# Performance work log

Hardware: AMD Instinct MI355X
Metric: run time of the kernel (lower is better)

## Reference

```python
import jax, jax.numpy as jnp
import numpy as np

HEAD_DIM = 128
N_HEADS = 32
N_KV_HEADS = 8
ROPE_BASE = 500000.0
QK_EPS = 1e-6


def _rope_cos_sin(position_ids, head_dim, base, dtype):
    # position_ids: [B, S] int -> cos/sin [B, 1, S, head_dim]
    inv_freq = 1.0 / (base ** (jnp.arange(0, head_dim, 2, dtype=jnp.float32) / head_dim))
    freqs = position_ids.astype(jnp.float32)[..., None] * inv_freq  # [B, S, D/2]
    emb = jnp.concatenate([freqs, freqs], axis=-1)  # [B, S, D]
    return jnp.cos(emb).astype(dtype)[:, None], jnp.sin(emb).astype(dtype)[:, None]


def _rotate_half(x):
    x1, x2 = jnp.split(x, 2, axis=-1)
    return jnp.concatenate([-x2, x1], axis=-1)


def _qk_norm(x, scale, eps):
    # L2 norm (not RMS): scale * x / (||x||_2 + eps)
    norm = jnp.sqrt(jnp.sum(x * x, axis=-1, keepdims=True))
    return scale * x / (norm + eps)


def setup_inputs() -> dict:
    key = jax.random.key(0)
    ks = jax.random.split(key, 7)
    B, S, H = 1, 2048, 4096
    kv_dim = N_KV_HEADS * HEAD_DIM
    return {
        "hidden_states": jax.random.normal(ks[0], (B, S, H), dtype=jnp.float32),
        "position_ids": jnp.broadcast_to(jnp.arange(S, dtype=jnp.int64 if jax.config.jax_enable_x64 else jnp.int32), (B, S)),
        "Wq": jax.random.normal(ks[1], (H, H), dtype=jnp.float32) * (H ** -0.5),
        "Wk": jax.random.normal(ks[2], (kv_dim, H), dtype=jnp.float32) * (H ** -0.5),
        "Wv": jax.random.normal(ks[3], (kv_dim, H), dtype=jnp.float32) * (H ** -0.5),
        "Wo": jax.random.normal(ks[4], (H, H), dtype=jnp.float32) * (H ** -0.5),
        "q_scale": jnp.ones((HEAD_DIM,), dtype=jnp.float32),
        "k_scale": jnp.ones((HEAD_DIM,), dtype=jnp.float32),
    }


def reference(hidden_states, position_ids, Wq, Wk, Wv, Wo, q_scale, k_scale):
    B, S, H = hidden_states.shape
    scaling = 1.0 / np.sqrt(HEAD_DIM)

    # projections (torch Linear: y = x @ W.T)
    q = (hidden_states @ Wq.T).reshape(B, S, N_HEADS, HEAD_DIM).transpose(0, 2, 1, 3)
    k = (hidden_states @ Wk.T).reshape(B, S, N_KV_HEADS, HEAD_DIM).transpose(0, 2, 1, 3)
    v = (hidden_states @ Wv.T).reshape(B, S, N_KV_HEADS, HEAD_DIM).transpose(0, 2, 1, 3)

    cos, sin = _rope_cos_sin(position_ids, HEAD_DIM, ROPE_BASE, q.dtype)
    q = q * cos + _rotate_half(q) * sin
    k = k * cos + _rotate_half(k) * sin

    q = _qk_norm(q, q_scale, QK_EPS)
    k = _qk_norm(k, k_scale, QK_EPS)

    # GQA: repeat kv heads to match query heads
    n_rep = N_HEADS // N_KV_HEADS
    k = jnp.repeat(k, n_rep, axis=1)  # [B, n_heads, S, D]
    v = jnp.repeat(v, n_rep, axis=1)

    # causal SDPA
    scores = jnp.einsum("bhqd,bhkd->bhqk", q, k) * scaling
    causal = jnp.tril(jnp.ones((S, S), dtype=bool))
    scores = jnp.where(causal, scores, jnp.finfo(scores.dtype).min)
    attn = jax.nn.softmax(scores, axis=-1)
    out = jnp.einsum("bhqk,bhkd->bhqd", attn, v)  # [B, H, S, D]

    out = out.transpose(0, 2, 1, 3).reshape(B, S, H)
    return out @ Wo.T
```

## Files before the change

### kernel.cpp

```cpp
#include <hip/hip_runtime.h>
#include <math.h>

typedef unsigned short u16;
typedef unsigned int u32;
typedef __attribute__((ext_vector_type(8))) short bf16x8;
typedef __attribute__((ext_vector_type(4))) float f32x4;

#define S_LEN 2048
#define HID 4096
#define NH 32
#define NKV 8
#define HD 128
#define QS 6144

__device__ __forceinline__ u16 f2bf(float f) {
  u32 u = __float_as_uint(f);
  u32 r = (u + 0x7FFFu + ((u >> 16) & 1u)) >> 16;
  return (u16)r;
}
__device__ __forceinline__ float bf2f(u16 v) {
  return __uint_as_float(((u32)v) << 16);
}
__device__ __forceinline__ f32x4 mfma16(bf16x8 a, bf16x8 b, f32x4 c) {
  return __builtin_amdgcn_mfma_f32_16x16x32_bf16(a, b, c, 0, 0, 0);
}
__device__ __forceinline__ void async16(const u16* g, u16* l) {
  __builtin_amdgcn_global_load_lds(
      (__attribute__((address_space(1))) void*)g,
      (__attribute__((address_space(3))) void*)l, 16, 0, 0);
}
#if __has_builtin(__builtin_amdgcn_exp2f)
#define EXP2(x) __builtin_amdgcn_exp2f(x)
#else
#define EXP2(x) exp2f(x)
#endif

__global__ __launch_bounds__(256) void conv_all(
    const float* __restrict__ hs, const float* __restrict__ wq,
    const float* __restrict__ wk, const float* __restrict__ wv,
    const float* __restrict__ wo, u16* __restrict__ dhs, u16* __restrict__ dwq,
    u16* __restrict__ dwk, u16* __restrict__ dwv, u16* __restrict__ dwo) {
  int i = blockIdx.x * 256 + threadIdx.x;
  const float* src;
  u16* dst;
  int off;
  if (i < 2097152) { src = hs; dst = dhs; off = 0; }
  else if (i < 6291456) { src = wq; dst = dwq; off = 2097152; }
  else if (i < 7340032) { src = wk; dst = dwk; off = 6291456; }
  else if (i < 8388608) { src = wv; dst = dwv; off = 7340032; }
  else { src = wo; dst = dwo; off = 8388608; }
  int j = i - off;
  float4 v = ((const float4*)src)[j];
  ushort4 o;
  o.x = f2bf(v.x); o.y = f2bf(v.y); o.z = f2bf(v.z); o.w = f2bf(v.w);
  ((ushort4*)dst)[j] = o;
}


#define VMC(n) asm volatile("s_waitcnt vmcnt(" #n ")" ::: "memory")

#define LDA(qi, d)                                                         \
  {                                                                        \
    const u16* p_ = As + (d)*16384 + (wm * 128 + (qi)*64 + cl) * 64;       \
    _Pragma("unroll") for (int ii = 0; ii < 4; ii++)                       \
        _Pragma("unroll") for (int kk = 0; kk < 2; kk++)                   \
            a0[ii][kk] =                                                   \
        *(const bf16x8*)(p_ + ii * 1024 + ((c0 ^ (kk << 2)) << 3));        \
  }

#define LDB(dst, qj, d)                                                    \
  {                                                                        \
    const u16* p_ = Bs + (d)*16384 + (wn * 64 + (qj)*32 + cl) * 64;        \
    _Pragma("unroll") for (int jj = 0; jj < 2; jj++)                       \
        _Pragma("unroll") for (int kk = 0; kk < 2; kk++)                   \
            dst[jj][kk] =                                                  \
        *(const bf16x8*)(p_ + jj * 1024 + ((c0 ^ (kk << 2)) << 3));        \
  }

#define MM(qi, qj, bsrc)                                                   \
  {                                                                        \
    _Pragma("unroll") for (int ii = 0; ii < 4; ii++)                       \
        _Pragma("unroll") for (int jj = 0; jj < 2; jj++)                   \
            _Pragma("unroll") for (int kk = 0; kk < 2; kk++)               \
                acc[(qi)*4 + ii][(qj)*2 + jj] =                            \
        mfma16(a0[ii][kk], bsrc[jj][kk], acc[(qi)*4 + ii][(qj)*2 + jj]);   \
  }

#define PH(MMA)                                                  \
  {                                                              \
    __builtin_amdgcn_s_barrier();                                \
    asm volatile("s_waitcnt lgkmcnt(0)" ::: "memory");           \
    __builtin_amdgcn_sched_barrier(0);                           \
    __builtin_amdgcn_s_setprio(1);                               \
    MMA;                                                         \
    __builtin_amdgcn_s_setprio(0);                               \
    __builtin_amdgcn_sched_barrier(0);                           \
    __builtin_amdgcn_s_barrier();                                \
  }

__global__ __launch_bounds__(512, 2) void gemm256(
    const u16* __restrict__ A, const u16* __restrict__ B,
    u16* __restrict__ Cb, float* __restrict__ Cf, int N, int K) {
  extern __shared__ u16 lds[];
  u16* As = lds;
  u16* Bs = lds + 32768;
  const int tid = threadIdx.x;
  const int lane = tid & 63, wv = tid >> 6;
  const int cl = lane & 15, qd = lane >> 4;
  const int wm = wv >> 2, wn = wv & 3;
  const int c0 = qd ^ (cl & 7);

  const int cpx = gridDim.x >> 3;
  const int swz = (blockIdx.x & 7) * cpx + (blockIdx.x >> 3);
  const int m0 = (swz & 7) * 256;
  const int n0 = (swz >> 3) * 256;

  u32 aof[2][2], bof[2][2];
#pragma unroll
  for (int h = 0; h < 2; h++)
#pragma unroll
    for (int q = 0; q < 2; q++) {
      int g = q * 512 + wv * 64 + lane;
      int r = h * 128 + (g >> 3);
      int c = (g & 7) ^ (r & 7);
      aof[h][q] = (u32)(m0 + r) * K + c * 8;
      bof[h][q] = (u32)(n0 + r) * K + c * 8;
    }
  u16* asb = As + wv * 512;
  u16* bsb = Bs + wv * 512;

  f32x4 acc[8][4];
  f32x4 zz = {0.f, 0.f, 0.f, 0.f};
#pragma unroll
  for (int i = 0; i < 8; i++)
#pragma unroll
    for (int j = 0; j < 4; j++) acc[i][j] = zz;
  bf16x8 a0[4][2], b0[2][2], b1[2][2];

  const int NT = K >> 6;

  {
    auto sh = [&](const u16* g, const u32* off, int t, u16* dst) {
      async16(g + (size_t)t * 64 + off[0], dst);
      async16(g + (size_t)t * 64 + off[1], dst + 4096);
    };
    sh(A, aof[0], 0, asb);
    sh(A, aof[1], 0, asb + 8192);
    sh(B, bof[0], 0, bsb);
    sh(B, bof[1], 0, bsb + 8192);
    sh(B, bof[0], 1, bsb + 16384);
    sh(B, bof[1], 1, bsb + 16384 + 8192);
  }
  VMC(4);
  __builtin_amdgcn_sched_barrier(0);
  __builtin_amdgcn_s_barrier();

  for (int it = 0; it < (NT >> 1); ++it) {
    const int t = it * 2;
    const bool s2 = (t + 2) < NT;
    auto sh = [&](const u16* g, const u32* off, int tt, u16* dst) {
      async16(g + (size_t)tt * 64 + off[0], dst);
      async16(g + (size_t)tt * 64 + off[1], dst + 4096);
    };
    LDA(0, 0); LDB(b0, 0, 0);
    sh(A, aof[0], t + 1, asb + 16384);
    PH(MM(0, 0, b0));
    LDB(b1, 1, 0);
    sh(A, aof[1], t + 1, asb + 16384 + 8192);
    PH(MM(0, 1, b1));
    LDA(1, 0);
    if (s2) sh(B, bof[0], t + 2, bsb);
    PH(MM(1, 0, b0));
    if (s2) {
      sh(B, bof[1], t + 2, bsb + 8192);
      VMC(4);
    } else {
      VMC(0);
    }
    PH(MM(1, 1, b1));
    LDA(0, 1); LDB(b0, 0, 1);
    if (s2) sh(A, aof[0], t + 2, asb);
    PH(MM(0, 0, b0));
    LDB(b1, 1, 1);
    if (s2) sh(A, aof[1], t + 2, asb + 8192);
    PH(MM(0, 1, b1));
    LDA(1, 1);
    if (s2) sh(B, bof[0], t + 3, bsb + 16384);
    PH(MM(1, 0, b0));
    if (s2) sh(B, bof[1], t + 3, bsb + 16384 + 8192);
    VMC(4);
    PH(MM(1, 1, b1));
  }

#pragma unroll
  for (int i = 0; i < 8; i++)
#pragma unroll
    for (int j = 0; j < 4; j++) {
      int row = m0 + wm * 128 + i * 16 + qd * 4;
      int col = n0 + wn * 64 + j * 16 + cl;
#pragma unroll
      for (int r = 0; r < 4; r++) {
        float v = acc[i][j][r];
        if (Cb) Cb[(size_t)(row + r) * N + col] = f2bf(v);
        else    Cf[(size_t)(row + r) * N + col] = v;
      }
    }
}

__global__ __launch_bounds__(256) void rope_l2norm(
    u16* __restrict__ x, const int* __restrict__ pos_ids,
    const float* __restrict__ scale, int hmask, int hshift, int stride) {
  const int lane = threadIdx.x & 63;
  const int wv = threadIdx.x >> 6;
  const int idx = blockIdx.x * 4 + wv;
  const int s = idx >> hshift;
  const int h = idx & hmask;
  u16* p = x + (size_t)s * stride + h * HD;
  const float pos = (float)pos_ids[s];
  const float inv = expf((float)lane * -0.20503692777194264f);
  float sn, cs;
  sincosf(pos * inv, &sn, &cs);
  float a = bf2f(p[lane]);
  float b = bf2f(p[lane + 64]);
  float ra = a * cs - b * sn;
  float rb = b * cs + a * sn;
  float ss = ra * ra + rb * rb;
#pragma unroll
  for (int off = 32; off >= 1; off >>= 1) ss += __shfl_xor(ss, off, 64);
  float rd = 1.0f / (sqrtf(ss) + 1e-6f);
  p[lane] = f2bf(scale[lane] * ra * rd);
  p[lane + 64] = f2bf(scale[lane + 64] * rb * rd);
}

__global__ __launch_bounds__(256) void transpose_v(const u16* __restrict__ v,
                                                   u16* __restrict__ vt) {
  __shared__ u16 t[64][65];
  const int r = threadIdx.x >> 6;
  const int c = threadIdx.x & 63;
  const int s0 = blockIdx.x * 64, d0 = blockIdx.y * 64;
#pragma unroll
  for (int i = 0; i < 16; i++) {
    int row = i * 4 + r;
    t[row][c] = v[(size_t)(s0 + row) * QS + d0 + c];
  }
  __syncthreads();
#pragma unroll
  for (int i = 0; i < 16; i++) {
    int row = i * 4 + r;
    vt[(size_t)(d0 + row) * S_LEN + s0 + c] = t[c][row];
  }
}

#define PLD 68

__global__ __launch_bounds__(512) void flash_attn(
    const u16* __restrict__ QKV, const u16* __restrict__ Vt,
    u16* __restrict__ O) {
  __shared__ u16 Ks[64 * 128];
  __shared__ u16 Vs[128 * 64];
  __shared__ u16 Ps[128 * PLD];
  const int tid = threadIdx.x;
  const int lane = tid & 63, wv = tid >> 6;
  const int cl = lane & 15, qd = lane >> 4;
  const int qbi = blockIdx.x, h = blockIdx.y;
  const int q0 = qbi * 128, kvh = h >> 2;
  const float es = 0.12751629240081506f;

  bf16x8 aQ[4];
  {
    const u16* qrow = QKV + (size_t)(q0 + wv * 16 + cl) * QS + h * HD + qd * 8;
#pragma unroll
    for (int kk = 0; kk < 4; kk++) aQ[kk] = *(const bf16x8*)(qrow + kk * 32);
  }

  f32x4 oacc[8];
  f32x4 zz = {0.f, 0.f, 0.f, 0.f};
#pragma unroll
  for (int n = 0; n < 8; n++) oacc[n] = zz;
  float lsum[4] = {0.f, 0.f, 0.f, 0.f};

  const u16* Kbase = QKV + 4096 + kvh * HD;
  const u16* Vbase = Vt + (size_t)kvh * HD * S_LEN;

  const int row_min = q0 + wv * 16;
  const int ktmax = 2 * qbi + 1;

  for (int kt = 0; kt <= ktmax; kt++) {
    __syncthreads();
#pragma unroll
    for (int q = 0; q < 2; q++) {
      int c = q * 512 + wv * 64 + lane;
      int kr = c >> 4, kg = (c & 15) ^ (kr & 15);
      async16(Kbase + (size_t)(kt * 64 + kr) * QS + kg * 8,
              Ks + (q * 512 + wv * 64) * 8);
      int vr = c >> 3, vg = (c & 7) ^ (vr & 7);
      async16(Vbase + (size_t)vr * S_LEN + kt * 64 + vg * 8,
              Vs + (q * 512 + wv * 64) * 8);
    }
    __syncthreads();

    if (kt * 64 <= row_min + 15) {
      f32x4 sacc[4];
#pragma unroll
      for (int j = 0; j < 4; j++) sacc[j] = zz;
#pragma unroll
      for (int j = 0; j < 4; j++) {
        int row = j * 16 + cl;
#pragma unroll
        for (int kk = 0; kk < 4; kk++) {
          int ch = (kk * 4 + qd) ^ (row & 15);
          bf16x8 bK = *(const bf16x8*)&Ks[row * 128 + ch * 8];
          sacc[j] = mfma16(aQ[kk], bK, sacc[j]);
        }
      }

      float pm[4][4];
      if (kt * 64 + 63 > row_min) {
        const int grow = row_min + qd * 4;
#pragma unroll
        for (int j = 0; j < 4; j++) {
          int gcol = kt * 64 + j * 16 + cl;
#pragma unroll
          for (int r = 0; r < 4; r++)
            pm[j][r] = (gcol <= grow + r) ? EXP2(sacc[j][r] * es) : 0.f;
        }
      } else {
#pragma unroll
        for (int j = 0; j < 4; j++)
#pragma unroll
          for (int r = 0; r < 4; r++) pm[j][r] = EXP2(sacc[j][r] * es);
      }
#pragma unroll
      for (int j = 0; j < 4; j++)
#pragma unroll
        for (int r = 0; r < 4; r++) lsum[r] += pm[j][r];

#pragma unroll
      for (int j = 0; j < 4; j++)
#pragma unroll
        for (int r = 0; r < 4; r++)
          Ps[(wv * 16 + qd * 4 + r) * PLD + j * 16 + cl] = f2bf(pm[j][r]);
      __asm__ volatile("s_waitcnt lgkmcnt(0)" ::: "memory");

#pragma unroll
      for (int kk = 0; kk < 2; kk++) {
        bf16x8 aP = *(const bf16x8*)&Ps[(wv * 16 + cl) * PLD + kk * 32 + qd * 8];
#pragma unroll
        for (int n = 0; n < 8; n++) {
          int row = n * 16 + cl;
          int ch = (kk * 4 + qd) ^ (row & 7);
          bf16x8 bV = *(const bf16x8*)&Vs[row * 64 + ch * 8];
          oacc[n] = mfma16(aP, bV, oacc[n]);
        }
      }
    }
  }

#pragma unroll
  for (int r = 0; r < 4; r++) {
#pragma unroll
    for (int off = 8; off >= 1; off >>= 1) lsum[r] += __shfl_xor(lsum[r], off, 64);
  }
#pragma unroll
  for (int r = 0; r < 4; r++) {
    float il = 1.0f / lsum[r];
    int row = row_min + qd * 4 + r;
#pragma unroll
    for (int n = 0; n < 8; n++)
      O[(size_t)row * HID + h * HD + n * 16 + cl] = f2bf(oacc[n][r] * il);
  }
}

extern "C" void kernel_launch(void* const* d_in, const int* in_sizes, int n_in,
                              void* d_out, int out_size, void* d_ws, size_t ws_size,
                              hipStream_t stream) {
  const float* hs = (const float*)d_in[0];
  const int* pos = (const int*)d_in[1];
  const float* Wq = (const float*)d_in[2];
  const float* Wk = (const float*)d_in[3];
  const float* Wv = (const float*)d_in[4];
  const float* Wo = (const float*)d_in[5];
  const float* qsc = (const float*)d_in[6];
  const float* ksc = (const float*)d_in[7];
  float* out = (float*)d_out;
  char* ws = (char*)d_ws;
  const size_t MB = 1u << 20;

  u16* hs_b  = (u16*)(ws + 0 * MB);
  u16* wq_b  = (u16*)(ws + 16 * MB);
  u16* wk_b  = (u16*)(ws + 48 * MB);
  u16* wv_b  = (u16*)(ws + 56 * MB);
  u16* qkv_b = (u16*)(ws + 64 * MB);
  u16* vt_b  = (u16*)(ws + 88 * MB);
  u16* wo_b  = (u16*)(ws + 92 * MB);
  u16* o_b   = hs_b;

  static bool attr_set = false;
  if (!attr_set) {
    hipFuncSetAttribute(reinterpret_cast<const void*>(gemm256),
                        hipFuncAttributeMaxDynamicSharedMemorySize, 131072);
    attr_set = true;
  }

  conv_all<<<49152, 256, 0, stream>>>(hs, Wq, Wk, Wv, Wo,
                                      hs_b, wq_b, wk_b, wv_b, wo_b);

  gemm256<<<dim3((S_LEN / 256) * (QS / 256)), 512, 131072, stream>>>(
      hs_b, wq_b, qkv_b, nullptr, QS, HID);

  rope_l2norm<<<S_LEN * NH / 4, 256, 0, stream>>>(qkv_b, pos, qsc, NH - 1, 5, QS);
  rope_l2norm<<<S_LEN * NKV / 4, 256, 0, stream>>>(qkv_b + 4096, pos, ksc, NKV - 1, 3, QS);
  transpose_v<<<dim3(S_LEN / 64, (NKV * HD) / 64), 256, 0, stream>>>(qkv_b + 5120, vt_b);

  flash_attn<<<dim3(S_LEN / 128, NH), 512, 0, stream>>>(qkv_b, vt_b, o_b);

  gemm256<<<dim3((S_LEN / 256) * (HID / 256)), 512, 131072, stream>>>(
      o_b, wo_b, nullptr, out, HID, HID);
}
```

Before: 516.8 us.

## Shrink GEMM tiles for more blocks and pair causal attention query blocks

The GEMM kernel is templated on N-tile width (256x192 for the QKV projection, 256x128 for the output projection) with a 4x2 wave layout. This raises the block count to fill more compute units and lowers LDS per block, at the cost of less data reuse per tile. Flash attention now runs each block over two query tiles, i and 15-i, so every block does the same causal amount of work. This removes the triangular load imbalance but halves the grid to 256 blocks.

```diff
diff --git a/kernel.cpp b/kernel.cpp
--- a/kernel.cpp
+++ b/kernel.cpp
@@ -61,8 +61,8 @@
 
 #define LDA(qi, d)                                                         \
   {                                                                        \
-    const u16* p_ = As + (d)*16384 + (wm * 128 + (qi)*64 + cl) * 64;       \
-    _Pragma("unroll") for (int ii = 0; ii < 4; ii++)                       \
+    const u16* p_ = As + (d)*16384 + (wm * 64 + (qi)*32 + cl) * 64;        \
+    _Pragma("unroll") for (int ii = 0; ii < 2; ii++)                       \
         _Pragma("unroll") for (int kk = 0; kk < 2; kk++)                   \
             a0[ii][kk] =                                                   \
         *(const bf16x8*)(p_ + ii * 1024 + ((c0 ^ (kk << 2)) << 3));        \
@@ -70,8 +70,9 @@
 
 #define LDB(dst, qj, d)                                                    \
   {                                                                        \
-    const u16* p_ = Bs + (d)*16384 + (wn * 64 + (qj)*32 + cl) * 64;        \
-    _Pragma("unroll") for (int jj = 0; jj < 2; jj++)                       \
+    const u16* p_ =                                                        \
+        Bs + (d)*BSTR + (wn * (BN / 2) + (qj) * (BN / 4) + cl) * 64;       \
+    _Pragma("unroll") for (int jj = 0; jj < NJ; jj++)                      \
         _Pragma("unroll") for (int kk = 0; kk < 2; kk++)                   \
             dst[jj][kk] =                                                  \
         *(const bf16x8*)(p_ + jj * 1024 + ((c0 ^ (kk << 2)) << 3));        \
@@ -79,11 +80,11 @@
 
 #define MM(qi, qj, bsrc)                                                   \
   {                                                                        \
-    _Pragma("unroll") for (int ii = 0; ii < 4; ii++)                       \
-        _Pragma("unroll") for (int jj = 0; jj < 2; jj++)                   \
+    _Pragma("unroll") for (int ii = 0; ii < 2; ii++)                       \
+        _Pragma("unroll") for (int jj = 0; jj < NJ; jj++)                  \
             _Pragma("unroll") for (int kk = 0; kk < 2; kk++)               \
-                acc[(qi)*4 + ii][(qj)*2 + jj] =                            \
-        mfma16(a0[ii][kk], bsrc[jj][kk], acc[(qi)*4 + ii][(qj)*2 + jj]);   \
+                acc[(qi)*2 + ii][(qj)*NJ + jj] = mfma16(                   \
+                    a0[ii][kk], bsrc[jj][kk], acc[(qi)*2 + ii][(qj)*NJ + jj]); \
   }
 
 #define PH(MMA)                                                  \
@@ -98,106 +99,116 @@
     __builtin_amdgcn_s_barrier();                                \
   }
 
-__global__ __launch_bounds__(512, 2) void gemm256(
+#define VMCNJ()                       \
+  {                                   \
+    if constexpr (NJ == 2) VMC(2);    \
+    else VMC(3);                      \
+  }
+
+template <int NJ>
+__global__ __launch_bounds__(512, 2) void gemm8p(
     const u16* __restrict__ A, const u16* __restrict__ B,
     u16* __restrict__ Cb, float* __restrict__ Cf, int N, int K) {
+  constexpr int BN = NJ * 64;
+  constexpr int BSTR = BN * 64;
   extern __shared__ u16 lds[];
   u16* As = lds;
   u16* Bs = lds + 32768;
   const int tid = threadIdx.x;
   const int lane = tid & 63, wv = tid >> 6;
   const int cl = lane & 15, qd = lane >> 4;
-  const int wm = wv >> 2, wn = wv & 3;
+  const int wm = wv >> 1, wn = wv & 1;
   const int c0 = qd ^ (cl & 7);
 
   const int cpx = gridDim.x >> 3;
   const int swz = (blockIdx.x & 7) * cpx + (blockIdx.x >> 3);
   const int m0 = (swz & 7) * 256;
-  const int n0 = (swz >> 3) * 256;
-
-  u32 aof[2][2], bof[2][2];
-#pragma unroll
-  for (int h = 0; h < 2; h++)
-#pragma unroll
-    for (int q = 0; q < 2; q++) {
-      int g = q * 512 + wv * 64 + lane;
-      int r = h * 128 + (g >> 3);
-      int c = (g & 7) ^ (r & 7);
-      aof[h][q] = (u32)(m0 + r) * K + c * 8;
-      bof[h][q] = (u32)(n0 + r) * K + c * 8;
-    }
-  u16* asb = As + wv * 512;
-  u16* bsb = Bs + wv * 512;
-
-  f32x4 acc[8][4];
+  const int n0 = (swz >> 3) * BN;
+
+  u32 aof[4], bof[NJ];
+#pragma unroll
+  for (int q = 0; q < 4; q++) {
+    int r = q * 64 + wv * 8 + (lane >> 3);
+    int c = (lane & 7) ^ (r & 7);
+    aof[q] = (u32)(m0 + r) * K + c * 8;
+  }
+#pragma unroll
+  for (int q = 0; q < NJ; q++) {
+    int r = q * 64 + wv * 8 + (lane >> 3);
+    int c = (lane & 7) ^ (r & 7);
+    bof[q] = (u32)(n0 + r) * K + c * 8;
+  }
+  const int sbo = wv * 512;
+
+  auto STA = [&](int t, int d, int ra) {
+    async16(A + (size_t)t * 64 + aof[ra], As + d * 16384 + ra * 4096 + sbo);
+  };
+  auto STB = [&](int t, int d, int rb) {
+    async16(B + (size_t)t * 64 + bof[rb], Bs + d * BSTR + rb * 4096 + sbo);
+  };
+
+  f32x4 acc[4][2 * NJ];
   f32x4 zz = {0.f, 0.f, 0.f, 0.f};
 #pragma unroll
-  for (int i = 0; i < 8; i++)
-#pragma unroll
-    for (int j = 0; j < 4; j++) acc[i][j] = zz;
-  bf16x8 a0[4][2], b0[2][2], b1[2][2];
+  for (int i = 0; i < 4; i++)
+#pragma unroll
+    for (int j = 0; j < 2 * NJ; j++) acc[i][j] = zz;
+  bf16x8 a0[2][2], b0[NJ][2], b1[NJ][2];
 
   const int NT = K >> 6;
 
-  {
-    auto sh = [&](const u16* g, const u32* off, int t, u16* dst) {
-      async16(g + (size_t)t * 64 + off[0], dst);
-      async16(g + (size_t)t * 64 + off[1], dst + 4096);
-    };
-    sh(A, aof[0], 0, asb);
-    sh(A, aof[1], 0, asb + 8192);
-    sh(B, bof[0], 0, bsb);
-    sh(B, bof[1], 0, bsb + 8192);
-    sh(B, bof[0], 1, bsb + 16384);
-    sh(B, bof[1], 1, bsb + 16384 + 8192);
-  }
-  VMC(4);
+  STA(0, 0, 0); STA(0, 0, 1); STA(0, 0, 2); STA(0, 0, 3);
+  STB(0, 0, 0); STB(0, 0, 1);
+  if constexpr (NJ == 3) STB(0, 0, 2);
+  STB(1, 1, 0); STB(1, 1, 1);
+  if constexpr (NJ == 3) STB(1, 1, 2);
+  VMCNJ();
   __builtin_amdgcn_sched_barrier(0);
   __builtin_amdgcn_s_barrier();
 
   for (int it = 0; it < (NT >> 1); ++it) {
     const int t = it * 2;
     const bool s2 = (t + 2) < NT;
-    auto sh = [&](const u16* g, const u32* off, int tt, u16* dst) {
-      async16(g + (size_t)tt * 64 + off[0], dst);
-      async16(g + (size_t)tt * 64 + off[1], dst + 4096);
-    };
     LDA(0, 0); LDB(b0, 0, 0);
-    sh(A, aof[0], t + 1, asb + 16384);
+    STA(t + 1, 1, 0); STA(t + 1, 1, 1);
     PH(MM(0, 0, b0));
     LDB(b1, 1, 0);
-    sh(A, aof[1], t + 1, asb + 16384 + 8192);
+    STA(t + 1, 1, 2); STA(t + 1, 1, 3);
     PH(MM(0, 1, b1));
     LDA(1, 0);
-    if (s2) sh(B, bof[0], t + 2, bsb);
+    if (s2) { STB(t + 2, 0, 0); STB(t + 2, 0, 1); }
     PH(MM(1, 0, b0));
     if (s2) {
-      sh(B, bof[1], t + 2, bsb + 8192);
-      VMC(4);
+      if constexpr (NJ == 3) STB(t + 2, 0, 2);
+      VMCNJ();
     } else {
       VMC(0);
     }
     PH(MM(1, 1, b1));
     LDA(0, 1); LDB(b0, 0, 1);
-    if (s2) sh(A, aof[0], t + 2, asb);
+    if (s2) { STA(t + 2, 0, 0); STA(t + 2, 0, 1); }
     PH(MM(0, 0, b0));
     LDB(b1, 1, 1);
-    if (s2) sh(A, aof[1], t + 2, asb + 8192);
+    if (s2) { STA(t + 2, 0, 2); STA(t + 2, 0, 3); }
     PH(MM(0, 1, b1));
     LDA(1, 1);
-    if (s2) sh(B, bof[0], t + 3, bsb + 16384);
+    if (s2) { STB(t + 3, 1, 0); STB(t + 3, 1, 1); }
     PH(MM(1, 0, b0));
-    if (s2) sh(B, bof[1], t + 3, bsb + 16384 + 8192);
-    VMC(4);
+    if (s2) {
+      if constexpr (NJ == 3) STB(t + 3, 1, 2);
+      VMCNJ();
+    } else {
+      VMC(0);
+    }
     PH(MM(1, 1, b1));
   }
 
 #pragma unroll
-  for (int i = 0; i < 8; i++)
-#pragma unroll
-    for (int j = 0; j < 4; j++) {
-      int row = m0 + wm * 128 + i * 16 + qd * 4;
-      int col = n0 + wn * 64 + j * 16 + cl;
+  for (int i = 0; i < 4; i++)
+#pragma unroll
+    for (int j = 0; j < 2 * NJ; j++) {
+      int row = m0 + wm * 64 + i * 16 + qd * 4;
+      int col = n0 + wn * (BN / 2) + (j / NJ) * (BN / 4) + (j % NJ) * 16 + cl;
 #pragma unroll
       for (int r = 0; r < 4; r++) {
         float v = acc[i][j][r];
@@ -262,112 +273,120 @@
   const int tid = threadIdx.x;
   const int lane = tid & 63, wv = tid >> 6;
   const int cl = lane & 15, qd = lane >> 4;
-  const int qbi = blockIdx.x, h = blockIdx.y;
-  const int q0 = qbi * 128, kvh = h >> 2;
+  const int h = blockIdx.y;
+  const int kvh = h >> 2;
   const float es = 0.12751629240081506f;
-
-  bf16x8 aQ[4];
-  {
-    const u16* qrow = QKV + (size_t)(q0 + wv * 16 + cl) * QS + h * HD + qd * 8;
-#pragma unroll
-    for (int kk = 0; kk < 4; kk++) aQ[kk] = *(const bf16x8*)(qrow + kk * 32);
-  }
-
-  f32x4 oacc[8];
-  f32x4 zz = {0.f, 0.f, 0.f, 0.f};
-#pragma unroll
-  for (int n = 0; n < 8; n++) oacc[n] = zz;
-  float lsum[4] = {0.f, 0.f, 0.f, 0.f};
 
   const u16* Kbase = QKV + 4096 + kvh * HD;
   const u16* Vbase = Vt + (size_t)kvh * HD * S_LEN;
 
-  const int row_min = q0 + wv * 16;
-  const int ktmax = 2 * qbi + 1;
-
-  for (int kt = 0; kt <= ktmax; kt++) {
-    __syncthreads();
-#pragma unroll
-    for (int q = 0; q < 2; q++) {
-      int c = q * 512 + wv * 64 + lane;
-      int kr = c >> 4, kg = (c & 15) ^ (kr & 15);
-      async16(Kbase + (size_t)(kt * 64 + kr) * QS + kg * 8,
-              Ks + (q * 512 + wv * 64) * 8);
-      int vr = c >> 3, vg = (c & 7) ^ (vr & 7);
-      async16(Vbase + (size_t)vr * S_LEN + kt * 64 + vg * 8,
-              Vs + (q * 512 + wv * 64) * 8);
-    }
-    __syncthreads();
-
-    if (kt * 64 <= row_min + 15) {
-      f32x4 sacc[4];
-#pragma unroll
-      for (int j = 0; j < 4; j++) sacc[j] = zz;
-#pragma unroll
-      for (int j = 0; j < 4; j++) {
-        int row = j * 16 + cl;
-#pragma unroll
-        for (int kk = 0; kk < 4; kk++) {
-          int ch = (kk * 4 + qd) ^ (row & 15);
-          bf16x8 bK = *(const bf16x8*)&Ks[row * 128 + ch * 8];
-          sacc[j] = mfma16(aQ[kk], bK, sacc[j]);
+  for (int half = 0; half < 2; half++) {
+    const int qbi = half ? (15 - blockIdx.x) : blockIdx.x;
+    const int q0 = qbi * 128;
+
+    bf16x8 aQ[4];
+    {
+      const u16* qrow =
+          QKV + (size_t)(q0 + wv * 16 + cl) * QS + h * HD + qd * 8;
+#pragma unroll
+      for (int kk = 0; kk < 4; kk++) aQ[kk] = *(const bf16x8*)(qrow + kk * 32);
+    }
+
+    f32x4 oacc[8];
+    f32x4 zz = {0.f, 0.f, 0.f, 0.f};
+#pragma unroll
+    for (int n = 0; n < 8; n++) oacc[n] = zz;
+    float lsum[4] = {0.f, 0.f, 0.f, 0.f};
+
+    const int row_min = q0 + wv * 16;
+    const int ktmax = 2 * qbi + 1;
+
+    for (int kt = 0; kt <= ktmax; kt++) {
+      __syncthreads();
+#pragma unroll
+      for (int q = 0; q < 2; q++) {
+        int c = q * 512 + wv * 64 + lane;
+        int kr = c >> 4, kg = (c & 15) ^ (kr & 15);
+        async16(Kbase + (size_t)(kt * 64 + kr) * QS + kg * 8,
+                Ks + (q * 512 + wv * 64) * 8);
+        int vr = c >> 3, vg = (c & 7) ^ (vr & 7);
+        async16(Vbase + (size_t)vr * S_LEN + kt * 64 + vg * 8,
+                Vs + (q * 512 + wv * 64) * 8);
+      }
+      __syncthreads();
+
+      if (kt * 64 <= row_min + 15) {
+        f32x4 sacc[4];
+#pragma unroll
+        for (int j = 0; j < 4; j++) sacc[j] = zz;
+#pragma unroll
+        for (int j = 0; j < 4; j++) {
+          int row = j * 16 + cl;
+#pragma unroll
+          for (int kk = 0; kk < 4; kk++) {
+            int ch = (kk * 4 + qd) ^ (row & 15);
+            bf16x8 bK = *(const bf16x8*)&Ks[row * 128 + ch * 8];
+            sacc[j] = mfma16(aQ[kk], bK, sacc[j]);
+          }
+        }
+
+        float pm[4][4];
+        if (kt * 64 + 63 > row_min) {
+          const int grow = row_min + qd * 4;
+#pragma unroll
+          for (int j = 0; j < 4; j++) {
+            int gcol = kt * 64 + j * 16 + cl;
+#pragma unroll
+            for (int r = 0; r < 4; r++)
+              pm[j][r] = (gcol <= grow + r) ? EXP2(sacc[j][r] * es) : 0.f;
+          }
+        } else {
+#pragma unroll
+          for (int j = 0; j < 4; j++)
+#pragma unroll
+            for (int r = 0; r < 4; r++) pm[j][r] = EXP2(sacc[j][r] * es);
+        }
+#pragma unroll
+        for (int j = 0; j < 4; j++)
+#pragma unroll
+          for (int r = 0; r < 4; r++) lsum[r] += pm[j][r];
+
+#pragma unroll
+        for (int j = 0; j < 4; j++)
+#pragma unroll
+          for (int r = 0; r < 4; r++)
+            Ps[(wv * 16 + qd * 4 + r) * PLD + j * 16 + cl] = f2bf(pm[j][r]);
+        __asm__ volatile("s_waitcnt lgkmcnt(0)" ::: "memory");
+
+#pragma unroll
+        for (int kk = 0; kk < 2; kk++) {
+          bf16x8 aP =
+              *(const bf16x8*)&Ps[(wv * 16 + cl) * PLD + kk * 32 + qd * 8];
+#pragma unroll
+          for (int n = 0; n < 8; n++) {
+            int row = n * 16 + cl;
+            int ch = (kk * 4 + qd) ^ (row & 7);
+            bf16x8 bV = *(const bf16x8*)&Vs[row * 64 + ch * 8];
+            oacc[n] = mfma16(aP, bV, oacc[n]);
+          }
         }
       }
-
-      float pm[4][4];
-      if (kt * 64 + 63 > row_min) {
-        const int grow = row_min + qd * 4;
-#pragma unroll
-        for (int j = 0; j < 4; j++) {
-          int gcol = kt * 64 + j * 16 + cl;
-#pragma unroll
-          for (int r = 0; r < 4; r++)
-            pm[j][r] = (gcol <= grow + r) ? EXP2(sacc[j][r] * es) : 0.f;
-        }
-      } else {
-#pragma unroll
-        for (int j = 0; j < 4; j++)
-#pragma unroll
-          for (int r = 0; r < 4; r++) pm[j][r] = EXP2(sacc[j][r] * es);
-      }
-#pragma unroll
-      for (int j = 0; j < 4; j++)
-#pragma unroll
-        for (int r = 0; r < 4; r++) lsum[r] += pm[j][r];
-
-#pragma unroll
-      for (int j = 0; j < 4; j++)
-#pragma unroll
-        for (int r = 0; r < 4; r++)
-          Ps[(wv * 16 + qd * 4 + r) * PLD + j * 16 + cl] = f2bf(pm[j][r]);
-      __asm__ volatile("s_waitcnt lgkmcnt(0)" ::: "memory");
-
-#pragma unroll
-      for (int kk = 0; kk < 2; kk++) {
-        bf16x8 aP = *(const bf16x8*)&Ps[(wv * 16 + cl) * PLD + kk * 32 + qd * 8];
-#pragma unroll
-        for (int n = 0; n < 8; n++) {
-          int row = n * 16 + cl;
-          int ch = (kk * 4 + qd) ^ (row & 7);
-          bf16x8 bV = *(const bf16x8*)&Vs[row * 64 + ch * 8];
-          oacc[n] = mfma16(aP, bV, oacc[n]);
-        }
-      }
-    }
-  }
-
-#pragma unroll
-  for (int r = 0; r < 4; r++) {
-#pragma unroll
-    for (int off = 8; off >= 1; off >>= 1) lsum[r] += __shfl_xor(lsum[r], off, 64);
-  }
-#pragma unroll
-  for (int r = 0; r < 4; r++) {
-    float il = 1.0f / lsum[r];
-    int row = row_min + qd * 4 + r;
-#pragma unroll
-    for (int n = 0; n < 8; n++)
-      O[(size_t)row * HID + h * HD + n * 16 + cl] = f2bf(oacc[n][r] * il);
+    }
+
+#pragma unroll
+    for (int r = 0; r < 4; r++) {
+#pragma unroll
+      for (int off = 8; off >= 1; off >>= 1)
+        lsum[r] += __shfl_xor(lsum[r], off, 64);
+    }
+#pragma unroll
+    for (int r = 0; r < 4; r++) {
+      float il = 1.0f / lsum[r];
+      int row = row_min + qd * 4 + r;
+#pragma unroll
+      for (int n = 0; n < 8; n++)
+        O[(size_t)row * HID + h * HD + n * 16 + cl] = f2bf(oacc[n][r] * il);
+    }
   }
 }
 
@@ -397,23 +416,25 @@
 
   static bool attr_set = false;
   if (!attr_set) {
-    hipFuncSetAttribute(reinterpret_cast<const void*>(gemm256),
-                        hipFuncAttributeMaxDynamicSharedMemorySize, 131072);
+    hipFuncSetAttribute(reinterpret_cast<const void*>(&gemm8p<3>),
+                        hipFuncAttributeMaxDynamicSharedMemorySize, 114688);
+    hipFuncSetAttribute(reinterpret_cast<const void*>(&gemm8p<2>),
+                        hipFuncAttributeMaxDynamicSharedMemorySize, 98304);
     attr_set = true;
   }
 
   conv_all<<<49152, 256, 0, stream>>>(hs, Wq, Wk, Wv, Wo,
                                       hs_b, wq_b, wk_b, wv_b, wo_b);
 
-  gemm256<<<dim3((S_LEN / 256) * (QS / 256)), 512, 131072, stream>>>(
+  gemm8p<3><<<dim3(8 * (QS / 192)), 512, 114688, stream>>>(
       hs_b, wq_b, qkv_b, nullptr, QS, HID);
 
   rope_l2norm<<<S_LEN * NH / 4, 256, 0, stream>>>(qkv_b, pos, qsc, NH - 1, 5, QS);
   rope_l2norm<<<S_LEN * NKV / 4, 256, 0, stream>>>(qkv_b + 4096, pos, ksc, NKV - 1, 3, QS);
   transpose_v<<<dim3(S_LEN / 64, (NKV * HD) / 64), 256, 0, stream>>>(qkv_b + 5120, vt_b);
 
-  flash_attn<<<dim3(S_LEN / 128, NH), 512, 0, stream>>>(qkv_b, vt_b, o_b);
-
-  gemm256<<<dim3((S_LEN / 256) * (HID / 256)), 512, 131072, stream>>>(
+  flash_attn<<<dim3(8, NH), 512, 0, stream>>>(qkv_b, vt_b, o_b);
+
+  gemm8p<2><<<dim3(8 * (HID / 128)), 512, 98304, stream>>>(
       o_b, wo_b, nullptr, out, HID, HID);
 }
```

After: 454.9 us. 1.14x faster.
